# Kernel optimization log

Measured on AMD Instinct MI355X. Metric: run time of the kernel, lower is better.

Reference implementation:

```python
import jax, jax.numpy as jnp
import numpy as np

B, L, D = 2, 2048, 2048
N, K, H = 16, 8, 128
EPS = 1e-6
ROPE_THETA = 1000000
K_MASK = -2.3819763e+38


def rms_norm(x, w, eps=EPS):
    dtype = x.dtype
    rms = jnp.sqrt(jnp.mean(x.astype(jnp.float32) ** 2, axis=-1, keepdims=True) + eps)
    return (w * x / rms).astype(dtype)


def apply_rope(inputs, positions, head_dim, rope_theta=ROPE_THETA):
    # inputs: [B, L, n, H], positions: [B, L]
    fraction = 2 * jnp.arange(0, head_dim // 2, dtype=jnp.float32) / head_dim
    timescale = rope_theta ** fraction  # [H/2]
    sinusoid = positions[..., jnp.newaxis] / timescale[jnp.newaxis, jnp.newaxis, :]  # [B,L,H/2]
    sinusoid = sinusoid[..., jnp.newaxis, :]  # [B,L,1,H/2]
    sin, cos = jnp.sin(sinusoid), jnp.cos(sinusoid)
    first, second = jnp.split(inputs, 2, axis=-1)
    out = jnp.concatenate([first * cos - second * sin, second * cos + first * sin], axis=-1)
    return out.astype(inputs.dtype)


def setup_inputs() -> dict:
    key = jax.random.key(0)
    ks = jax.random.split(key, 6)
    x = jax.random.normal(ks[0], (B, L, D), dtype=jnp.float32)
    position_ids = jnp.broadcast_to(jnp.arange(L, dtype=jnp.int32)[None, :], (B, L))
    # causal mask [B, L, S]
    attn_mask = jnp.broadcast_to(jnp.tril(jnp.ones((L, L), dtype=bool))[None], (B, L, L))
    wq = jax.random.normal(ks[1], (D, N, H), dtype=jnp.float32) * 0.02
    wk = jax.random.normal(ks[2], (D, K, H), dtype=jnp.float32) * 0.02
    wv = jax.random.normal(ks[3], (D, K, H), dtype=jnp.float32) * 0.02
    wo = jax.random.normal(ks[4], (N, H, D), dtype=jnp.float32) * 0.02
    q_norm_w = jnp.ones((H,), dtype=jnp.float32)
    k_norm_w = jnp.ones((H,), dtype=jnp.float32)
    return {"x": x, "position_ids": position_ids, "attn_mask": attn_mask,
            "wq": wq, "wk": wk, "wv": wv, "wo": wo,
            "q_norm_w": q_norm_w, "k_norm_w": k_norm_w}


def reference(x, position_ids, attn_mask, wq, wk, wv, wo, q_norm_w, k_norm_w):
    scale = H ** (-0.5)
    q = jnp.einsum('BLD,DNH->BLNH', x, wq)  # [B,L,N,H]
    k = jnp.einsum('BSD,DKH->BSKH', x, wk)  # [B,S,K,H]
    v = jnp.einsum('BSD,DKH->BSKH', x, wv)
    q = rms_norm(q, q_norm_w)
    k = rms_norm(k, k_norm_w)
    q = apply_rope(q, position_ids, H)
    k = apply_rope(k, position_ids, H)
    b, l, n, h = q.shape
    s = k.shape[1]
    kk = k.shape[2]
    q = q.reshape((b, l, kk, n // kk, h))
    attn = jnp.einsum('BLKGH,BSKH->BKGLS', q, k) * scale
    attn = attn.reshape((b, n, l, s))
    attn = jnp.where(jnp.expand_dims(attn_mask, -3), attn, K_MASK)
    attn = jax.nn.softmax(attn.astype(jnp.float32), axis=-1).astype(k.dtype)
    attn = attn.reshape((b, kk, n // kk, l, s))
    qkv = jnp.einsum('BKGLS,BSKH->BLKGH', attn, v).reshape((b, l, n, h))
    out = jnp.einsum('BLNH,NHD->BLD', qkv, wo)
    return out
```

## Files before the change

### kernel.cpp

```cpp
#include <hip/hip_runtime.h>

#define B_ 2
#define L_ 2048
#define D_ 2048
#define NH_ 16
#define KH_ 8
#define HD_ 128

typedef __attribute__((ext_vector_type(8))) short short8;
typedef __attribute__((ext_vector_type(4))) float floatx4;

__device__ __forceinline__ unsigned short f2bf(float f) {
  unsigned u = __float_as_uint(f);
  unsigned r = (u + 0x7fffu + ((u >> 16) & 1u)) >> 16;
  return (unsigned short)r;
}
__device__ __forceinline__ float bf2f(unsigned short h) {
  return __uint_as_float(((unsigned)h) << 16);
}
__device__ __forceinline__ void gl_lds16(const void* g, void* l) {
  __builtin_amdgcn_global_load_lds(
      (const __attribute__((address_space(1))) unsigned int*)g,
      (__attribute__((address_space(3))) unsigned int*)l, 16, 0, 0);
}

__global__ __launch_bounds__(256) void cvt_f32_bf16(const float* __restrict__ in,
                                                    unsigned short* __restrict__ out) {
  long i = ((long)blockIdx.x * 256 + threadIdx.x) * 4;
  float4 v = *(const float4*)(in + i);
  ushort4 o;
  o.x = f2bf(v.x); o.y = f2bf(v.y); o.z = f2bf(v.z); o.w = f2bf(v.w);
  *(ushort4*)(out + i) = o;
}

__global__ __launch_bounds__(256) void transpose_cvt(const float* __restrict__ in,
                                                     unsigned short* __restrict__ out,
                                                     int R, int C, int ostride) {
  __shared__ float tile[32][33];
  int c0 = blockIdx.x * 32, r0 = blockIdx.y * 32;
  int tx = threadIdx.x, ty = threadIdx.y;
#pragma unroll
  for (int i = 0; i < 4; i++)
    tile[ty + i * 8][tx] = in[(long)(r0 + ty + i * 8) * C + c0 + tx];
  __syncthreads();
#pragma unroll
  for (int i = 0; i < 4; i++) {
    int oc = ty + i * 8;
    out[(long)(c0 + oc) * ostride + r0 + tx] = f2bf(tile[tx][oc]);
  }
}

__global__ __launch_bounds__(256) void transpose_v(const unsigned short* __restrict__ qkv,
                                                   unsigned short* __restrict__ vT) {
  __shared__ unsigned short tile[32][33];
  int l0 = blockIdx.x * 32, h0 = blockIdx.y * 32;
  int bk = blockIdx.z;
  int b = bk >> 3, kh = bk & 7;
  int tx = threadIdx.x, ty = threadIdx.y;
  const unsigned short* src = qkv + (long)b * L_ * 4096 + 3072 + kh * 128;
#pragma unroll
  for (int i = 0; i < 4; i++)
    tile[ty + i * 8][tx] = src[(long)(l0 + ty + i * 8) * 4096 + h0 + tx];
  __syncthreads();
  unsigned short* dst = vT + (long)bk * HD_ * L_;
#pragma unroll
  for (int i = 0; i < 4; i++)
    dst[(long)(h0 + ty + i * 8) * L_ + l0 + tx] = tile[tx][ty + i * 8];
}

template <int OUT_BF16>
__global__ __launch_bounds__(256, 2) void gemm128(const unsigned short* __restrict__ A,
                                                  const unsigned short* __restrict__ Bt,
                                                  void* __restrict__ C,
                                                  int M, int N, int K) {
  __shared__ unsigned short As[128 * 64];
  __shared__ unsigned short Bs[128 * 64];
  const int t = threadIdx.x;
  const int lane = t & 63, w = t >> 6;
  const int wy = w >> 1, wx = w & 1;
  const int col = lane & 15, quad = lane >> 4;
  const long m0 = (long)blockIdx.y * 128, n0 = (long)blockIdx.x * 128;
  floatx4 acc[4][4];
#pragma unroll
  for (int i = 0; i < 4; i++)
#pragma unroll
    for (int j = 0; j < 4; j++) acc[i][j] = (floatx4)0.0f;
  const int rs = t >> 3, bs = t & 7;
  for (int kt = 0; kt < K; kt += 64) {
#pragma unroll
    for (int i = 0; i < 4; i++) {
      int r = i * 32 + rs;
      gl_lds16(A + (m0 + r) * (long)K + kt + ((bs ^ (r & 7)) << 3),
               &As[(i * 32 + w * 8) * 64]);
      gl_lds16(Bt + (n0 + r) * (long)K + kt + ((bs ^ (r & 7)) << 3),
               &Bs[(i * 32 + w * 8) * 64]);
    }
    __syncthreads();
#pragma unroll
    for (int ks = 0; ks < 2; ks++) {
      short8 af[4], bf[4];
#pragma unroll
      for (int mi = 0; mi < 4; mi++) {
        int row = wy * 64 + mi * 16 + col;
        int blk = ks * 4 + quad;
        af[mi] = *(const short8*)&As[row * 64 + ((blk ^ (row & 7)) << 3)];
      }
#pragma unroll
      for (int ni = 0; ni < 4; ni++) {
        int row = wx * 64 + ni * 16 + col;
        int blk = ks * 4 + quad;
        bf[ni] = *(const short8*)&Bs[row * 64 + ((blk ^ (row & 7)) << 3)];
      }
#pragma unroll
      for (int mi = 0; mi < 4; mi++)
#pragma unroll
        for (int ni = 0; ni < 4; ni++)
          acc[mi][ni] = __builtin_amdgcn_mfma_f32_16x16x32_bf16(af[mi], bf[ni],
                                                                acc[mi][ni], 0, 0, 0);
    }
    __syncthreads();
  }
#pragma unroll
  for (int mi = 0; mi < 4; mi++)
#pragma unroll
    for (int r = 0; r < 4; r++) {
      long row = m0 + wy * 64 + mi * 16 + quad * 4 + r;
#pragma unroll
      for (int ni = 0; ni < 4; ni++) {
        long cg = n0 + wx * 64 + ni * 16 + col;
        float val = acc[mi][ni][r];
        if (OUT_BF16)
          ((unsigned short*)C)[row * N + cg] = f2bf(val);
        else
          ((float*)C)[row * N + cg] = val;
      }
    }
}

__global__ __launch_bounds__(256) void rmsrope(const unsigned short* __restrict__ qkv,
                                               const int* __restrict__ pos,
                                               const float* __restrict__ qw,
                                               const float* __restrict__ kw,
                                               unsigned short* __restrict__ qo,
                                               unsigned short* __restrict__ ko) {
  const int t = threadIdx.x, lane = t & 63, w = t >> 6;
  const int gid = blockIdx.x * 4 + w;
  const int row = gid / 24;
  const int hd = gid - row * 24;
  const int b = row >> 11, l = row & 2047;
  const unsigned short* src = qkv + (long)row * 4096 + hd * 128;
  float x0 = bf2f(src[lane]);
  float x1 = bf2f(src[lane + 64]);
  float ss = x0 * x0 + x1 * x1;
#pragma unroll
  for (int off = 32; off; off >>= 1) ss += __shfl_xor(ss, off);
  float inv = 1.0f / sqrtf(ss * (1.0f / 128.0f) + 1e-6f);
  const float* nw = (hd < 16) ? qw : kw;
  x0 = nw[lane] * x0 * inv;
  x1 = nw[lane + 64] * x1 * inv;
  float p = (float)pos[row];
  float ts = powf(1.0e6f, (float)lane * (1.0f / 64.0f));
  float ang = p / ts;
  float s, c;
  sincosf(ang, &s, &c);
  float o0 = x0 * c - x1 * s;
  float o1 = x1 * c + x0 * s;
  unsigned short* dst;
  if (hd < 16) {
    const float QSC = 0.08838834764831845f * 1.4426950408889634f;
    o0 *= QSC;
    o1 *= QSC;
    dst = qo + (((long)b * NH_ + hd) * L_ + l) * HD_;
  } else {
    dst = ko + (((long)b * KH_ + (hd - 16)) * L_ + l) * HD_;
  }
  dst[lane] = f2bf(o0);
  dst[lane + 64] = f2bf(o1);
}

__global__ __launch_bounds__(256, 2) void flash(const unsigned short* __restrict__ Q,
                                                const unsigned short* __restrict__ Kg,
                                                const unsigned short* __restrict__ VT,
                                                unsigned short* __restrict__ Og) {
  __shared__ unsigned short Ks[64 * 128];
  __shared__ unsigned short Vs[128 * 64];
  __shared__ unsigned short Ps[128 * 72];
  const int n = blockIdx.y, b = blockIdx.z;
  const int qt = b ? (15 - blockIdx.x) : blockIdx.x;
  const int t = threadIdx.x, lane = t & 63, w = t >> 6;
  const int col = lane & 15, quad = lane >> 4;
  const int kvh = n >> 1;
  const unsigned short* kb = Kg + ((long)b * KH_ + kvh) * L_ * HD_;
  const unsigned short* vtb = VT + ((long)b * KH_ + kvh) * HD_ * L_;
  const int l0 = qt * 128;
  const int steps = 2 * qt + 2;
  const unsigned short* qb = Q + (((long)b * NH_ + n) * L_ + l0) * HD_;

  short8 qf[2][4];
#pragma unroll
  for (int mi = 0; mi < 2; mi++)
#pragma unroll
    for (int ks = 0; ks < 4; ks++)
      qf[mi][ks] = *(const short8*)(qb + (w * 32 + mi * 16 + col) * 128 + ks * 32 + quad * 8);

  floatx4 o[2][8];
#pragma unroll
  for (int mi = 0; mi < 2; mi++)
#pragma unroll
    for (int nf = 0; nf < 8; nf++) o[mi][nf] = (floatx4)0.0f;
  float lrow[2][4];
#pragma unroll
  for (int mi = 0; mi < 2; mi++)
#pragma unroll
    for (int r = 0; r < 4; r++) lrow[mi][r] = 0.0f;

  for (int st = 0; st < steps; st++) {
    const int s0 = st * 64;
    {
      const int rK = t >> 4, blkK = t & 15;
#pragma unroll
      for (int i = 0; i < 4; i++) {
        int r = i * 16 + rK;
        int gblk = (blkK & 8) | ((blkK ^ r) & 7);
        gl_lds16(kb + (long)(s0 + r) * 128 + gblk * 8, &Ks[(i * 16 + w * 4) * 128]);
      }
    }
    {
      const int rV = t >> 3, blkV = t & 7;
#pragma unroll
      for (int j = 0; j < 4; j++) {
        int r = j * 32 + rV;
        int gblk = (blkV ^ r) & 7;
        gl_lds16(vtb + (long)r * L_ + s0 + gblk * 8, &Vs[(j * 32 + w * 8) * 64]);
      }
    }
    __syncthreads();

    floatx4 sa[2][4];
#pragma unroll
    for (int mi = 0; mi < 2; mi++)
#pragma unroll
      for (int sf = 0; sf < 4; sf++) sa[mi][sf] = (floatx4)0.0f;
#pragma unroll
    for (int ks = 0; ks < 4; ks++) {
      short8 bf[4];
#pragma unroll
      for (int sf = 0; sf < 4; sf++) {
        int srow = sf * 16 + col;
        int blk = ks * 4 + quad;
        bf[sf] = *(const short8*)&Ks[srow * 128 + (((blk & 8) | ((blk ^ srow) & 7)) << 3)];
      }
#pragma unroll
      for (int mi = 0; mi < 2; mi++)
#pragma unroll
        for (int sf = 0; sf < 4; sf++)
          sa[mi][sf] = __builtin_amdgcn_mfma_f32_16x16x32_bf16(qf[mi][ks], bf[sf],
                                                               sa[mi][sf], 0, 0, 0);
    }

    if (st >= steps - 2) {
#pragma unroll
      for (int mi = 0; mi < 2; mi++)
#pragma unroll
        for (int sf = 0; sf < 4; sf++)
#pragma unroll
          for (int r = 0; r < 4; r++) {
            int lr = l0 + w * 32 + mi * 16 + quad * 4 + r;
            int sr = s0 + sf * 16 + col;
            if (sr > lr) sa[mi][sf][r] = -3.0e38f;
          }
    }

#pragma unroll
    for (int mi = 0; mi < 2; mi++)
#pragma unroll
      for (int sf = 0; sf < 4; sf++)
#pragma unroll
        for (int r = 0; r < 4; r++) {
          float pv = exp2f(sa[mi][sf][r] - 17.0f);
          sa[mi][sf][r] = pv;
          lrow[mi][r] += pv;
        }

#pragma unroll
    for (int mi = 0; mi < 2; mi++)
#pragma unroll
      for (int sf = 0; sf < 4; sf++)
#pragma unroll
        for (int r = 0; r < 4; r++)
          Ps[(w * 32 + mi * 16 + quad * 4 + r) * 72 + sf * 16 + col] = f2bf(sa[mi][sf][r]);

#pragma unroll
    for (int ks = 0; ks < 2; ks++) {
      short8 pf[2];
#pragma unroll
      for (int mi = 0; mi < 2; mi++)
        pf[mi] = *(const short8*)&Ps[(w * 32 + mi * 16 + col) * 72 + ks * 32 + quad * 8];
      short8 vf[8];
#pragma unroll
      for (int nf = 0; nf < 8; nf++) {
        int h = nf * 16 + col;
        int blk = ks * 4 + quad;
        vf[nf] = *(const short8*)&Vs[h * 64 + ((blk ^ (h & 7)) << 3)];
      }
#pragma unroll
      for (int mi = 0; mi < 2; mi++)
#pragma unroll
        for (int nf = 0; nf < 8; nf++)
          o[mi][nf] = __builtin_amdgcn_mfma_f32_16x16x32_bf16(pf[mi], vf[nf],
                                                              o[mi][nf], 0, 0, 0);
    }
    __syncthreads();
  }

#pragma unroll
  for (int mi = 0; mi < 2; mi++)
#pragma unroll
    for (int r = 0; r < 4; r++) {
      float s = lrow[mi][r];
#pragma unroll
      for (int off = 8; off; off >>= 1) s += __shfl_xor(s, off);
      float inv = 1.0f / s;
      int lg = l0 + w * 32 + mi * 16 + quad * 4 + r;
      unsigned short* dst = Og + (((long)b * L_ + lg) * NH_ + n) * HD_;
#pragma unroll
      for (int nf = 0; nf < 8; nf++)
        dst[nf * 16 + col] = f2bf(o[mi][nf][r] * inv);
    }
}

extern "C" void kernel_launch(void* const* d_in, const int* in_sizes, int n_in,
                              void* d_out, int out_size, void* d_ws, size_t ws_size,
                              hipStream_t stream) {
  const float* x = (const float*)d_in[0];
  const int* pos = (const int*)d_in[1];
  const float* wq = (const float*)d_in[3];
  const float* wk = (const float*)d_in[4];
  const float* wv = (const float*)d_in[5];
  const float* wo = (const float*)d_in[6];
  const float* qnw = (const float*)d_in[7];
  const float* knw = (const float*)d_in[8];
  float* out = (float*)d_out;

  char* ws = (char*)d_ws;
  unsigned short* xb     = (unsigned short*)(ws + 0);
  unsigned short* wqkv_t = (unsigned short*)(ws + 16777216);
  unsigned short* wo_t   = (unsigned short*)(ws + 33554432);
  unsigned short* qkv    = (unsigned short*)(ws + 41943040);
  unsigned short* q      = (unsigned short*)(ws + 75497472);
  unsigned short* k      = (unsigned short*)(ws + 92274688);
  unsigned short* vT     = (unsigned short*)(ws + 100663296);
  unsigned short* ao     = (unsigned short*)(ws + 109051904);
  if (ws_size < 125829120) return;

  cvt_f32_bf16<<<8192, 256, 0, stream>>>(x, xb);
  dim3 tb(32, 8);
  transpose_cvt<<<dim3(64, 64), tb, 0, stream>>>(wq, wqkv_t, 2048, 2048, 2048);
  transpose_cvt<<<dim3(32, 64), tb, 0, stream>>>(wk, wqkv_t + 2048L * 2048, 2048, 1024, 2048);
  transpose_cvt<<<dim3(32, 64), tb, 0, stream>>>(wv, wqkv_t + 3072L * 2048, 2048, 1024, 2048);
  transpose_cvt<<<dim3(64, 64), tb, 0, stream>>>(wo, wo_t, 2048, 2048, 2048);
  gemm128<1><<<dim3(32, 32), 256, 0, stream>>>(xb, wqkv_t, qkv, 4096, 4096, 2048);
  rmsrope<<<24576, 256, 0, stream>>>(qkv, pos, qnw, knw, q, k);
  transpose_v<<<dim3(64, 4, 16), tb, 0, stream>>>(qkv, vT);
  flash<<<dim3(16, NH_, B_), 256, 0, stream>>>(q, k, vT, ao);
  gemm128<0><<<dim3(16, 32), 256, 0, stream>>>(ao, wo_t, out, 4096, 2048, 2048);
}
```

Baseline: 393.5 us.

## Merge weight transposes, alias P buffer onto K tile, raise flash occupancy

Folds the four weight transpose launches into one kernel that dispatches on block index. In the flash kernel, the P tile now reuses the K shared-memory buffer with an XOR-swizzled layout, which needs an extra barrier after the QK MFMAs. It also raises the launch bound to four blocks per CU and uses reversed tile order for both batches. The RoPE timescale is computed with exp2f instead of powf and a division. The intent is to cut launch overhead and shared-memory use so more flash blocks fit per CU, at the cost of an extra sync and possible register pressure.

```diff
diff --git a/kernel.cpp b/kernel.cpp
--- a/kernel.cpp
+++ b/kernel.cpp
@@ -33,11 +33,27 @@
   *(ushort4*)(out + i) = o;
 }
 
-__global__ __launch_bounds__(256) void transpose_cvt(const float* __restrict__ in,
-                                                     unsigned short* __restrict__ out,
-                                                     int R, int C, int ostride) {
+__global__ __launch_bounds__(256) void transpose_all(const float* __restrict__ wq,
+                                                     const float* __restrict__ wk,
+                                                     const float* __restrict__ wv,
+                                                     const float* __restrict__ wo,
+                                                     unsigned short* __restrict__ wqkv_t,
+                                                     unsigned short* __restrict__ wo_t) {
   __shared__ float tile[32][33];
-  int c0 = blockIdx.x * 32, r0 = blockIdx.y * 32;
+  int id = blockIdx.x;
+  const float* in;
+  unsigned short* out;
+  int C, sh;
+  if (id < 4096) {
+    in = wq; out = wqkv_t; C = 2048; sh = 6;
+  } else if (id < 6144) {
+    in = wk; out = wqkv_t + 2048L * 2048; C = 1024; sh = 5; id -= 4096;
+  } else if (id < 8192) {
+    in = wv; out = wqkv_t + 3072L * 2048; C = 1024; sh = 5; id -= 6144;
+  } else {
+    in = wo; out = wo_t; C = 2048; sh = 6; id -= 8192;
+  }
+  int c0 = (id & ((1 << sh) - 1)) * 32, r0 = (id >> sh) * 32;
   int tx = threadIdx.x, ty = threadIdx.y;
 #pragma unroll
   for (int i = 0; i < 4; i++)
@@ -46,7 +62,7 @@
 #pragma unroll
   for (int i = 0; i < 4; i++) {
     int oc = ty + i * 8;
-    out[(long)(c0 + oc) * ostride + r0 + tx] = f2bf(tile[tx][oc]);
+    out[(long)(c0 + oc) * 2048 + r0 + tx] = f2bf(tile[tx][oc]);
   }
 }
 
@@ -159,8 +175,7 @@
   x0 = nw[lane] * x0 * inv;
   x1 = nw[lane + 64] * x1 * inv;
   float p = (float)pos[row];
-  float ts = powf(1.0e6f, (float)lane * (1.0f / 64.0f));
-  float ang = p / ts;
+  float ang = p * exp2f((float)lane * -0.31143075889f);
   float s, c;
   sincosf(ang, &s, &c);
   float o0 = x0 * c - x1 * s;
@@ -178,15 +193,15 @@
   dst[lane + 64] = f2bf(o1);
 }
 
-__global__ __launch_bounds__(256, 2) void flash(const unsigned short* __restrict__ Q,
+__global__ __launch_bounds__(256, 4) void flash(const unsigned short* __restrict__ Q,
                                                 const unsigned short* __restrict__ Kg,
                                                 const unsigned short* __restrict__ VT,
                                                 unsigned short* __restrict__ Og) {
   __shared__ unsigned short Ks[64 * 128];
   __shared__ unsigned short Vs[128 * 64];
-  __shared__ unsigned short Ps[128 * 72];
+  unsigned short* Ps = Ks;
   const int n = blockIdx.y, b = blockIdx.z;
-  const int qt = b ? (15 - blockIdx.x) : blockIdx.x;
+  const int qt = 15 - blockIdx.x;
   const int t = threadIdx.x, lane = t & 63, w = t >> 6;
   const int col = lane & 15, quad = lane >> 4;
   const int kvh = n >> 1;
@@ -257,6 +272,7 @@
           sa[mi][sf] = __builtin_amdgcn_mfma_f32_16x16x32_bf16(qf[mi][ks], bf[sf],
                                                                sa[mi][sf], 0, 0, 0);
     }
+    __syncthreads();
 
     if (st >= steps - 2) {
 #pragma unroll
@@ -278,24 +294,21 @@
 #pragma unroll
         for (int r = 0; r < 4; r++) {
           float pv = exp2f(sa[mi][sf][r] - 17.0f);
-          sa[mi][sf][r] = pv;
           lrow[mi][r] += pv;
+          int prow = w * 32 + mi * 16 + quad * 4 + r;
+          int scol = sf * 16 + col;
+          Ps[prow * 64 + (((scol >> 3) ^ (prow & 7)) << 3) + (scol & 7)] = f2bf(pv);
         }
-
-#pragma unroll
-    for (int mi = 0; mi < 2; mi++)
-#pragma unroll
-      for (int sf = 0; sf < 4; sf++)
-#pragma unroll
-        for (int r = 0; r < 4; r++)
-          Ps[(w * 32 + mi * 16 + quad * 4 + r) * 72 + sf * 16 + col] = f2bf(sa[mi][sf][r]);
 
 #pragma unroll
     for (int ks = 0; ks < 2; ks++) {
       short8 pf[2];
 #pragma unroll
-      for (int mi = 0; mi < 2; mi++)
-        pf[mi] = *(const short8*)&Ps[(w * 32 + mi * 16 + col) * 72 + ks * 32 + quad * 8];
+      for (int mi = 0; mi < 2; mi++) {
+        int prow = w * 32 + mi * 16 + col;
+        int blk = ks * 4 + quad;
+        pf[mi] = *(const short8*)&Ps[prow * 64 + ((blk ^ (prow & 7)) << 3)];
+      }
       short8 vf[8];
 #pragma unroll
       for (int nf = 0; nf < 8; nf++) {
@@ -355,10 +368,7 @@
 
   cvt_f32_bf16<<<8192, 256, 0, stream>>>(x, xb);
   dim3 tb(32, 8);
-  transpose_cvt<<<dim3(64, 64), tb, 0, stream>>>(wq, wqkv_t, 2048, 2048, 2048);
-  transpose_cvt<<<dim3(32, 64), tb, 0, stream>>>(wk, wqkv_t + 2048L * 2048, 2048, 1024, 2048);
-  transpose_cvt<<<dim3(32, 64), tb, 0, stream>>>(wv, wqkv_t + 3072L * 2048, 2048, 1024, 2048);
-  transpose_cvt<<<dim3(64, 64), tb, 0, stream>>>(wo, wo_t, 2048, 2048, 2048);
+  transpose_all<<<12288, tb, 0, stream>>>(wq, wk, wv, wo, wqkv_t, wo_t);
   gemm128<1><<<dim3(32, 32), 256, 0, stream>>>(xb, wqkv_t, qkv, 4096, 4096, 2048);
   rmsrope<<<24576, 256, 0, stream>>>(qkv, pos, qnw, knw, q, k);
   transpose_v<<<dim3(64, 4, 16), tb, 0, stream>>>(qkv, vT);
```

Measured after the change: 761.6 us. +93.6%, slower.
